# Performance work log

Measured on AMD Instinct MI355X. Metric: run time of the kernel, lower is better.

## Reference

```python
import jax, jax.numpy as jnp
import numpy as np

G, B, T, H = 14, 64, 2048, 6  # nb_gaussians, batch, track_len, nb_hidden_variables
LOG_2PI = float(np.log(2.0 * np.pi))


def _dnn(x, d):
    # tf.math.divide_no_nan, safe under autodiff
    d_safe = jnp.where(d == 0, 1.0, d)
    return jnp.where(d == 0, 0.0, x / d_safe)


def _norm_log_gaussian(t):
    return -0.5 * (LOG_2PI + t ** 2)


def _gaussian_product(c1, c2, n1, n2, b1, b2, k):
    # RNN_gaussian_product: combine gaussians 1,2 so output-3 no longer depends
    # on coef k and output-4 carries it. (Tiny 1e-20/1e-100 TF noise terms are
    # numerically void and omitted.)
    C1 = c1[:, :, k:k + 1]  # [B,T,1]
    C2 = c2[:, :, k:k + 1]
    cc1, cc2 = _dnn(c1, C1), _dnn(c2, C2)
    nn1, nn2 = _dnn(n1, C1), _dnn(n2, C2)
    bb1, bb2 = _dnn(b1, C1[:, :, 0]), _dnn(b2, C2[:, :, 0])
    var1 = 1.0 / C1 ** 2
    var2 = 1.0 / C2 ** 2
    var3 = var1 + var2
    std3 = jnp.sqrt(var3)
    c3 = (cc1 - cc2) / std3
    n3 = (nn1 - nn2) / std3
    b3 = (bb1 - bb2) / std3[:, :, 0]
    var4 = var1 * var2 / var3
    std4 = jnp.sqrt(var4)
    den = var3 * std4
    c4 = (cc1 * var2 + cc2 * var1) / den
    n4 = (nn1 * var2 + nn2 * var1) / den
    b4 = (bb1 * var2[:, :, 0] + bb2 * var1[:, :, 0]) / den[:, :, 0]
    logC = -jnp.log(jnp.abs(C1 * C2 * std4 * std3))[:, :, 0]
    return logC, c3, c4, n3, n4, b3, b4


def _forward(cur, nxt, biases):
    nH = cur.shape[-1]
    cur_l = list(cur)
    nxt_l = list(nxt)
    b_l = list(biases)
    LC = jnp.zeros(cur.shape[1:3], cur.dtype)  # [B,T]
    # Phase 1: integrate out each current hidden variable k.
    for k in range(nH):
        n = len(b_l)
        for i in range(n - 1):
            logC, c3, c4, n3, n4, b3, b4 = _gaussian_product(
                cur_l[i], cur_l[i + 1], nxt_l[i], nxt_l[i + 1], b_l[i], b_l[i + 1], k)
            cur_l[i], cur_l[i + 1] = c3, c4
            nxt_l[i], nxt_l[i + 1] = n3, n4
            b_l[i], b_l[i + 1] = b3, b4
            LC = LC + logC
        # final_RNN_function_phase_1: integrate & drop last dependent gaussian
        LC = LC - jnp.log(jnp.abs(cur_l[n - 1][:, :, k]))
        cur_l.pop(n - 1)
        nxt_l.pop(n - 1)
        b_l.pop(n - 1)
    # Phase 2: roles of current/next swapped; pop dependent gaussian into kept.
    kept_n, kept_b = [], []
    for k in range(nH):
        n = len(b_l)
        for i in range(n - 1):
            logC, n3, n4, c3, c4, b3, b4 = _gaussian_product(
                nxt_l[i], nxt_l[i + 1], cur_l[i], cur_l[i + 1], b_l[i], b_l[i + 1], k)
            nxt_l[i], nxt_l[i + 1] = n3, n4
            cur_l[i], cur_l[i + 1] = c3, c4
            b_l[i], b_l[i + 1] = b3, b4
            LC = LC + logC
        kept_n.append(nxt_l.pop(n - 1))
        kept_b.append(b_l.pop(n - 1))
        cur_l.pop(n - 1)
    # Remaining gaussians are pure constants
    LC = LC + jnp.sum(_norm_log_gaussian(jnp.stack(b_l)), axis=0)
    return jnp.stack(kept_n), jnp.stack(kept_b), LC


def setup_inputs() -> dict:
    key = jax.random.key(0)
    ks = jax.random.split(key, 5)

    def coefs(k1, k2, shape):
        mag = jax.random.uniform(k1, shape, jnp.float32, 0.5, 1.5)
        sgn = jnp.where(jax.random.bernoulli(k2, 0.5, shape), 1.0, -1.0)
        return mag * sgn

    cur = coefs(ks[0], ks[1], (G, B, T, H))
    nxt = coefs(ks[2], ks[3], (G, B, T, H))
    biases = jax.random.normal(ks[4], (G, B, T), jnp.float32)
    return {"current_hidden_var_coefs": cur,
            "next_hidden_var_coefs": nxt,
            "biases": biases}


def reference(current_hidden_var_coefs, next_hidden_var_coefs, biases):
    return _forward(current_hidden_var_coefs, next_hidden_var_coefs, biases)
```

## Files before the change

kernel.cpp:

```cpp
#include <hip/hip_runtime.h>

#define Gc 14
#define Hc 6
#define NPc (64*2048)
#define LOG_2PI 1.8378770664093453f

typedef float v2f __attribute__((ext_vector_type(2)));

__device__ __forceinline__ float frsq(float x){ return __builtin_amdgcn_rsqf(x); }
__device__ __forceinline__ float frcp(float x){ return __builtin_amdgcn_rcpf(x); }

template<int CTRL>
__device__ __forceinline__ float dppf(float x){
    union { float f; int i; } u; u.f = x;
    u.i = __builtin_amdgcn_update_dpp(0, u.i, CTRL, 0xF, 0xF, true);
    return u.f;
}
template<int L>
__device__ __forceinline__ float qbcast(float x){ return dppf<L * 0x55>(x); }

__device__ __forceinline__ void nt_store_v2f(float* p, v2f v){
    union { v2f f; unsigned long long u; } c; c.f = v;
    __builtin_nontemporal_store(c.u, (unsigned long long*)p);
}

template<int L, int B, int C, int N, bool UPD_LAST>
__device__ __forceinline__ float hh_sweep(v2f (&st)[Gc][2], float* sOut){
    float q0 = 0.f, q1 = 0.f;
    v2f d0 = {0.f, 0.f}, d1 = {0.f, 0.f};
    float hl = 0.f;
#pragma unroll
    for (int i = 0; i < N; ++i){
        const float hi = qbcast<L>(st[i][B][C]);
        if (i & 1) q1 = fmaf(hi, hi, q1); else q0 = fmaf(hi, hi, q0);
        const v2f H = {hi, hi};
        d0 = __builtin_elementwise_fma(H, st[i][0], d0);
        d1 = __builtin_elementwise_fma(H, st[i][1], d1);
        if (i == N - 1) hl = hi;
    }
    const float q    = q0 + q1;
    const float rn   = q * frsq(q);
    const float s    = copysignf(rn, hl);
    const float vl   = hl + s;
    const float beta = frcp(fmaf(s, hl, q));
    {
        const v2f S2 = {s, s};
        d0 = __builtin_elementwise_fma(S2, st[N - 1][0], d0);
        d1 = __builtin_elementwise_fma(S2, st[N - 1][1], d1);
    }
    const v2f B2 = {beta, beta};
    const v2f t0 = d0 * B2, t1 = d1 * B2;
#pragma unroll
    for (int i = 0; i < N - 1; ++i){
        const float hi = qbcast<L>(st[i][B][C]);
        const v2f Hn = {-hi, -hi};
        st[i][0] = __builtin_elementwise_fma(t0, Hn, st[i][0]);
        st[i][1] = __builtin_elementwise_fma(t1, Hn, st[i][1]);
    }
    if (UPD_LAST){
        const v2f Vn = {-vl, -vl};
        st[N - 1][0] = __builtin_elementwise_fma(t0, Vn, st[N - 1][0]);
        st[N - 1][1] = __builtin_elementwise_fma(t1, Vn, st[N - 1][1]);
    }
    *sOut = s;
    return rn;
}

__global__ void __launch_bounds__(256, 4)
gaussmerge_kernel(const float* __restrict__ cur_in,
                  const float* __restrict__ nxt_in,
                  const float* __restrict__ b_in,
                  float* __restrict__ out)
{
    const int tid = threadIdx.x;
    const int l = tid & 3;
    const int p = blockIdx.x * 64 + (tid >> 2);

    const float* arr   = (l < 2) ? cur_in : nxt_in;
    const float* baseA = arr + (size_t)p * Hc + ((l & 1) ? 2 : 0);
    const float* baseB = arr + (size_t)p * Hc + 4;
    const float* bp    = b_in + p;

    v2f st[Gc][2];
#pragma unroll
    for (int g = 0; g < Gc; ++g){
        const v2f A = *(const v2f*)(baseA + (size_t)g * (NPc * Hc));
        const v2f M = *(const v2f*)(baseB + (size_t)g * (NPc * Hc));
        const float bv = bp[(size_t)g * NPc];
        st[g][0] = A;
        st[g][1] = (l & 1) ? (v2f){bv, bv} : M;
    }

    float LC = 0.0f;
    float sdump;

    LC -= __logf(hh_sweep<0, 0, 0, 14, false>(st, &sdump));
    LC -= __logf(hh_sweep<0, 0, 1, 13, false>(st, &sdump));
    LC -= __logf(hh_sweep<1, 0, 0, 12, false>(st, &sdump));
    LC -= __logf(hh_sweep<1, 0, 1, 11, false>(st, &sdump));
    LC -= __logf(hh_sweep<0, 1, 0, 10, false>(st, &sdump));
    LC -= __logf(hh_sweep<0, 1, 1,  9, false>(st, &sdump));

    float* outN = out;
    float* outB = out + (size_t)Hc * NPc * Hc;
    float* outL = outB + (size_t)Hc * NPc;

#define PH2(K, L_, B_, C_, N_)                                                  \
    {                                                                           \
        float s_;                                                               \
        (void)hh_sweep<L_, B_, C_, N_, true>(st, &s_);                          \
        constexpr int m = (N_) - 1;                                             \
        const float flip = -copysignf(1.0f, s_);                                \
        const v2f F = {flip, flip};                                             \
        float* o = outN + (size_t)(K) * (NPc * Hc) + (size_t)p * Hc;            \
        if (l == 2){                                                            \
            nt_store_v2f(o,     st[m][0] * F);                    \
            nt_store_v2f(o + 4, st[m][1] * F);                    \
        } else if (l == 3){                                                     \
            nt_store_v2f(o + 2, st[m][0] * F);                    \
        } else if (l == 1){                                                     \
            __builtin_nontemporal_store(st[m][1][0] * flip,                     \
                                        outB + (size_t)(K) * NPc + p);          \
        }                                                                       \
    }

    PH2(0, 2, 0, 0, 8)
    PH2(1, 2, 0, 1, 7)
    PH2(2, 3, 0, 0, 6)
    PH2(3, 3, 0, 1, 5)
    PH2(4, 2, 1, 0, 4)
    PH2(5, 2, 1, 1, 3)
#undef PH2

    const float b0 = qbcast<1>(st[0][1][0]);
    const float b1 = qbcast<1>(st[1][1][0]);
    LC += -0.5f * (LOG_2PI + b0 * b0);
    LC += -0.5f * (LOG_2PI + b1 * b1);
    if (l == 0) __builtin_nontemporal_store(LC, outL + p);
}

extern "C" void kernel_launch(void* const* d_in, const int* in_sizes, int n_in,
                              void* d_out, int out_size, void* d_ws, size_t ws_size,
                              hipStream_t stream) {
    const float* cur = (const float*)d_in[0];
    const float* nxt = (const float*)d_in[1];
    const float* bia = (const float*)d_in[2];
    float* out = (float*)d_out;

    dim3 grid((NPc * 4) / 256), block(256);
    gaussmerge_kernel<<<grid, block, 0, stream>>>(cur, nxt, bia, out);
}
```

Baseline: 31.10 us.

## Repartition per-lane state to three coefs plus bias, dropping packed v2f math

```diff
diff --git a/kernel.cpp b/kernel.cpp
--- a/kernel.cpp
+++ b/kernel.cpp
@@ -4,8 +4,6 @@
 #define Hc 6
 #define NPc (64*2048)
 #define LOG_2PI 1.8378770664093453f
-
-typedef float v2f __attribute__((ext_vector_type(2)));
 
 __device__ __forceinline__ float frsq(float x){ return __builtin_amdgcn_rsqf(x); }
 __device__ __forceinline__ float frcp(float x){ return __builtin_amdgcn_rcpf(x); }
@@ -19,23 +17,23 @@
 template<int L>
 __device__ __forceinline__ float qbcast(float x){ return dppf<L * 0x55>(x); }
 
-__device__ __forceinline__ void nt_store_v2f(float* p, v2f v){
-    union { v2f f; unsigned long long u; } c; c.f = v;
-    __builtin_nontemporal_store(c.u, (unsigned long long*)p);
+__device__ __forceinline__ void nt_store_f(float* p, float v){
+    __builtin_nontemporal_store(v, p);
 }
 
-template<int L, int B, int C, int N, bool UPD_LAST>
-__device__ __forceinline__ float hh_sweep(v2f (&st)[Gc][2], float* sOut){
+template<int L, int B, int N, bool UPD_LAST>
+__device__ __forceinline__ float hh_sweep(float (&st)[Gc][4], float* sOut){
     float q0 = 0.f, q1 = 0.f;
-    v2f d0 = {0.f, 0.f}, d1 = {0.f, 0.f};
+    float d0 = 0.f, d1 = 0.f, d2 = 0.f, d3 = 0.f;
     float hl = 0.f;
 #pragma unroll
     for (int i = 0; i < N; ++i){
-        const float hi = qbcast<L>(st[i][B][C]);
+        const float hi = qbcast<L>(st[i][B]);
         if (i & 1) q1 = fmaf(hi, hi, q1); else q0 = fmaf(hi, hi, q0);
-        const v2f H = {hi, hi};
-        d0 = __builtin_elementwise_fma(H, st[i][0], d0);
-        d1 = __builtin_elementwise_fma(H, st[i][1], d1);
+        d0 = fmaf(hi, st[i][0], d0);
+        d1 = fmaf(hi, st[i][1], d1);
+        d2 = fmaf(hi, st[i][2], d2);
+        d3 = fmaf(hi, st[i][3], d3);
         if (i == N - 1) hl = hi;
     }
     const float q    = q0 + q1;
@@ -43,24 +41,24 @@
     const float s    = copysignf(rn, hl);
     const float vl   = hl + s;
     const float beta = frcp(fmaf(s, hl, q));
-    {
-        const v2f S2 = {s, s};
-        d0 = __builtin_elementwise_fma(S2, st[N - 1][0], d0);
-        d1 = __builtin_elementwise_fma(S2, st[N - 1][1], d1);
-    }
-    const v2f B2 = {beta, beta};
-    const v2f t0 = d0 * B2, t1 = d1 * B2;
+    d0 = fmaf(s, st[N - 1][0], d0);
+    d1 = fmaf(s, st[N - 1][1], d1);
+    d2 = fmaf(s, st[N - 1][2], d2);
+    d3 = fmaf(s, st[N - 1][3], d3);
+    const float t0 = d0 * beta, t1 = d1 * beta, t2 = d2 * beta, t3 = d3 * beta;
 #pragma unroll
     for (int i = 0; i < N - 1; ++i){
-        const float hi = qbcast<L>(st[i][B][C]);
-        const v2f Hn = {-hi, -hi};
-        st[i][0] = __builtin_elementwise_fma(t0, Hn, st[i][0]);
-        st[i][1] = __builtin_elementwise_fma(t1, Hn, st[i][1]);
+        const float hn = -qbcast<L>(st[i][B]);
+        st[i][0] = fmaf(t0, hn, st[i][0]);
+        st[i][1] = fmaf(t1, hn, st[i][1]);
+        st[i][2] = fmaf(t2, hn, st[i][2]);
+        st[i][3] = fmaf(t3, hn, st[i][3]);
     }
     if (UPD_LAST){
-        const v2f Vn = {-vl, -vl};
-        st[N - 1][0] = __builtin_elementwise_fma(t0, Vn, st[N - 1][0]);
-        st[N - 1][1] = __builtin_elementwise_fma(t1, Vn, st[N - 1][1]);
+        st[N - 1][0] = fmaf(t0, -vl, st[N - 1][0]);
+        st[N - 1][1] = fmaf(t1, -vl, st[N - 1][1]);
+        st[N - 1][2] = fmaf(t2, -vl, st[N - 1][2]);
+        st[N - 1][3] = fmaf(t3, -vl, st[N - 1][3]);
     }
     *sOut = s;
     return rn;
@@ -76,67 +74,70 @@
     const int l = tid & 3;
     const int p = blockIdx.x * 64 + (tid >> 2);
 
-    const float* arr   = (l < 2) ? cur_in : nxt_in;
-    const float* baseA = arr + (size_t)p * Hc + ((l & 1) ? 2 : 0);
-    const float* baseB = arr + (size_t)p * Hc + 4;
-    const float* bp    = b_in + p;
+    const float* arr  = (l < 2) ? cur_in : nxt_in;
+    const float* base = arr + (size_t)p * Hc + ((l & 1) ? 3 : 0);
+    const float* bp   = b_in + p;
 
-    v2f st[Gc][2];
+    float st[Gc][4];
 #pragma unroll
     for (int g = 0; g < Gc; ++g){
-        const v2f A = *(const v2f*)(baseA + (size_t)g * (NPc * Hc));
-        const v2f M = *(const v2f*)(baseB + (size_t)g * (NPc * Hc));
-        const float bv = bp[(size_t)g * NPc];
-        st[g][0] = A;
-        st[g][1] = (l & 1) ? (v2f){bv, bv} : M;
+        const float* rec = base + (size_t)g * (NPc * Hc);
+        if (l & 1){
+            const float  a = rec[0];
+            const float2 v = *(const float2*)(rec + 1);
+            st[g][0] = a; st[g][1] = v.x; st[g][2] = v.y;
+        } else {
+            const float2 v = *(const float2*)rec;
+            st[g][0] = v.x; st[g][1] = v.y; st[g][2] = rec[2];
+        }
+        st[g][3] = bp[(size_t)g * NPc];
     }
 
     float LC = 0.0f;
     float sdump;
 
-    LC -= __logf(hh_sweep<0, 0, 0, 14, false>(st, &sdump));
-    LC -= __logf(hh_sweep<0, 0, 1, 13, false>(st, &sdump));
-    LC -= __logf(hh_sweep<1, 0, 0, 12, false>(st, &sdump));
-    LC -= __logf(hh_sweep<1, 0, 1, 11, false>(st, &sdump));
-    LC -= __logf(hh_sweep<0, 1, 0, 10, false>(st, &sdump));
-    LC -= __logf(hh_sweep<0, 1, 1,  9, false>(st, &sdump));
+    LC -= __logf(hh_sweep<0, 0, 14, false>(st, &sdump));
+    LC -= __logf(hh_sweep<0, 1, 13, false>(st, &sdump));
+    LC -= __logf(hh_sweep<0, 2, 12, false>(st, &sdump));
+    LC -= __logf(hh_sweep<1, 0, 11, false>(st, &sdump));
+    LC -= __logf(hh_sweep<1, 1, 10, false>(st, &sdump));
+    LC -= __logf(hh_sweep<1, 2,  9, false>(st, &sdump));
 
     float* outN = out;
     float* outB = out + (size_t)Hc * NPc * Hc;
     float* outL = outB + (size_t)Hc * NPc;
 
-#define PH2(K, L_, B_, C_, N_)                                                  \
+#define PH2(K, L_, B_, N_)                                                      \
     {                                                                           \
         float s_;                                                               \
-        (void)hh_sweep<L_, B_, C_, N_, true>(st, &s_);                          \
+        (void)hh_sweep<L_, B_, N_, true>(st, &s_);                              \
         constexpr int m = (N_) - 1;                                             \
-        const float flip = -copysignf(1.0f, s_);                                \
-        const v2f F = {flip, flip};                                             \
+        const float flip = -copysignf(1.0f, s_);  \
         float* o = outN + (size_t)(K) * (NPc * Hc) + (size_t)p * Hc;            \
-        if (l == 2){                                                            \
-            nt_store_v2f(o,     st[m][0] * F);                    \
-            nt_store_v2f(o + 4, st[m][1] * F);                    \
-        } else if (l == 3){                                                     \
-            nt_store_v2f(o + 2, st[m][0] * F);                    \
-        } else if (l == 1){                                                     \
-            __builtin_nontemporal_store(st[m][1][0] * flip,                     \
-                                        outB + (size_t)(K) * NPc + p);          \
+        if (l == 2){                                            \
+            nt_store_f(o,     st[m][0] * flip);                                 \
+            nt_store_f(o + 1, st[m][1] * flip);                                 \
+            nt_store_f(o + 2, st[m][2] * flip);                                 \
+        } else if (l == 3){                                     \
+            nt_store_f(o + 3, st[m][0] * flip);                                 \
+            nt_store_f(o + 4, st[m][1] * flip);                                 \
+            nt_store_f(o + 5, st[m][2] * flip);                                 \
+        } else if (l == 1){                     \
+            nt_store_f(outB + (size_t)(K) * NPc + p, st[m][3] * flip);          \
         }                                                                       \
     }
 
-    PH2(0, 2, 0, 0, 8)
-    PH2(1, 2, 0, 1, 7)
-    PH2(2, 3, 0, 0, 6)
-    PH2(3, 3, 0, 1, 5)
-    PH2(4, 2, 1, 0, 4)
-    PH2(5, 2, 1, 1, 3)
+    PH2(0, 2, 0, 8)
+    PH2(1, 2, 1, 7)
+    PH2(2, 2, 2, 6)
+    PH2(3, 3, 0, 5)
+    PH2(4, 3, 1, 4)
+    PH2(5, 3, 2, 3)
 #undef PH2
 
-    const float b0 = qbcast<1>(st[0][1][0]);
-    const float b1 = qbcast<1>(st[1][1][0]);
-    LC += -0.5f * (LOG_2PI + b0 * b0);
-    LC += -0.5f * (LOG_2PI + b1 * b1);
-    if (l == 0) __builtin_nontemporal_store(LC, outL + p);
+    LC += -0.5f * (LOG_2PI + st[0][3] * st[0][3]);
+    LC += -0.5f * (LOG_2PI + st[1][3] * st[1][3]);
+    if (l == 0) nt_store_f(outL + p, LC);
 }
 
 extern "C" void kernel_launch(void* const* d_in, const int* in_sizes, int n_in,
```

New measurement: 29.47 us. 5.2% less time.
